# Optimization experiments

Measured on AMD Instinct MI355X. Metric: run time of the kernel, lower is better.

Reference implementation:

```python
import jax, jax.numpy as jnp
import numpy as np

B, L, D_IN, D_H, D_OUT = 8, 1024, 1024, 1024, 1024


def setup_inputs() -> dict:
    key = jax.random.key(0)
    ks = jax.random.split(key, 9)
    s = 0.02  # weight scale to keep ReLU chain stable
    return {
        "leaves": jax.random.normal(ks[0], (B, L, D_IN), dtype=jnp.float32),
        "V_w": jax.random.normal(ks[1], (D_H, D_IN), dtype=jnp.float32) * s,
        "V_b": jax.random.normal(ks[2], (D_H,), dtype=jnp.float32) * s,
        "U_w": jax.random.normal(ks[3], (D_H, D_H), dtype=jnp.float32) * s,
        "U_b": jax.random.normal(ks[4], (D_H,), dtype=jnp.float32) * s,
        "W_w": jax.random.normal(ks[5], (D_H, D_H), dtype=jnp.float32) * s,
        "W_b": jax.random.normal(ks[6], (D_H,), dtype=jnp.float32) * s,
        "O_w": jax.random.normal(ks[7], (D_OUT, D_H), dtype=jnp.float32) * s,
        "O_b": jax.random.normal(ks[8], (D_OUT,), dtype=jnp.float32) * s,
    }


def reference(leaves, V_w, V_b, U_w, U_b, W_w, W_b, O_w, O_b):
    # Leaf encoding: h_leaf = relu(V(x))            [B, L, H]
    h = jax.nn.relu(jnp.einsum("bli,hi->blh", leaves, V_w) + V_b)
    # Depth-batched recursion over the complete binary tree:
    # combined = relu(U(left) + W(right)); log2(L) levels, node count halves.
    while h.shape[1] > 1:
        left, right = h[:, 0::2], h[:, 1::2]  # [B, n/2, H] each
        h = jax.nn.relu(
            jnp.einsum("bnh,gh->bng", left, U_w) + U_b
            + jnp.einsum("bnh,gh->bng", right, W_w) + W_b
        )
    root = h[:, 0]  # [B, H]
    logits = jnp.einsum("bh,oh->bo", root, O_w) + O_b
    return jax.nn.log_softmax(logits, axis=-1)
```

## Files before the change

### kernel.cpp

```cpp
#include <hip/hip_runtime.h>
#include <hip/hip_bf16.h>
#include <math.h>

typedef __bf16 bf16_t;
typedef __bf16 bf16x8 __attribute__((ext_vector_type(8)));
typedef __bf16 bf16x4 __attribute__((ext_vector_type(4)));
typedef float  f32x4  __attribute__((ext_vector_type(4)));

#define GLD_LDS16(g, l)                                                          \
  __builtin_amdgcn_global_load_lds((const __attribute__((address_space(1))) void*)(g), \
                                   (__attribute__((address_space(3))) void*)(l), 16, 0, 0)

__global__ __launch_bounds__(256) void k_cvt_all(const float* __restrict__ leaves,
                                                 const float* __restrict__ V_w,
                                                 const float* __restrict__ O_w,
                                                 const float* __restrict__ U_w,
                                                 const float* __restrict__ W_w,
                                                 const float* __restrict__ U_b,
                                                 const float* __restrict__ W_b,
                                                 bf16_t* __restrict__ leaves_bf,
                                                 bf16_t* __restrict__ Vw_bf,
                                                 bf16_t* __restrict__ Ow_bf,
                                                 bf16_t* __restrict__ UW_bf,
                                                 float* __restrict__ buw) {
  const int gtid = blockIdx.x * 256 + threadIdx.x;
  const int G = gridDim.x * 256;
  for (int i = gtid; i < 2097152; i += G) {
    float4 v = reinterpret_cast<const float4*>(leaves)[i];
    bf16x4 o; o[0] = (bf16_t)v.x; o[1] = (bf16_t)v.y; o[2] = (bf16_t)v.z; o[3] = (bf16_t)v.w;
    reinterpret_cast<bf16x4*>(leaves_bf)[i] = o;
  }
  for (int i = gtid; i < 262144; i += G) {
    float4 v = reinterpret_cast<const float4*>(V_w)[i];
    bf16x4 o; o[0] = (bf16_t)v.x; o[1] = (bf16_t)v.y; o[2] = (bf16_t)v.z; o[3] = (bf16_t)v.w;
    reinterpret_cast<bf16x4*>(Vw_bf)[i] = o;
  }
  for (int i = gtid; i < 262144; i += G) {
    float4 v = reinterpret_cast<const float4*>(O_w)[i];
    bf16x4 o; o[0] = (bf16_t)v.x; o[1] = (bf16_t)v.y; o[2] = (bf16_t)v.z; o[3] = (bf16_t)v.w;
    reinterpret_cast<bf16x4*>(Ow_bf)[i] = o;
  }
  for (int idx = gtid; idx < 524288; idx += G) {
    int i = idx * 4;
    int g = i >> 11;
    int k = i & 2047;
    const float* src = (k < 1024) ? (U_w + g * 1024 + k) : (W_w + g * 1024 + (k - 1024));
    float4 v = *reinterpret_cast<const float4*>(src);
    bf16x4 o; o[0] = (bf16_t)v.x; o[1] = (bf16_t)v.y; o[2] = (bf16_t)v.z; o[3] = (bf16_t)v.w;
    reinterpret_cast<bf16x4*>(UW_bf)[idx] = o;
  }
  if (gtid < 1024) buw[gtid] = U_b[gtid] + W_b[gtid];
}

template <int TM, int TN, bool SPLIT>
__global__ __launch_bounds__(256, (TM == 128 ? 2 : 3)) void k_gemm(
    const bf16_t* __restrict__ A, const bf16_t* __restrict__ Bw,
    const float* __restrict__ bias, bf16_t* __restrict__ C,
    bf16_t* __restrict__ P, int M, int Kstride, int kchunk) {
  constexpr int MI = TM / 32;
  constexpr int NJ = TN / 32;
  constexpr int VM = TM / 64 + TN / 64;
  constexpr int NB = (TM == 128 ? 5 : 4);
  __shared__ bf16_t As[NB][TM * 32];
  __shared__ bf16_t Bs[NB][TN * 32];

  const int tid = threadIdx.x;
  const int lane = tid & 63;
  const int wave = tid >> 6;
  const int wr = wave >> 1, wc = wave & 1;
  const int bm = blockIdx.x, bn = blockIdx.y, bz = blockIdx.z;

  const bf16_t* Abase = A + (size_t)bm * TM * Kstride + (size_t)bz * kchunk;
  const bf16_t* Bbase = Bw + (size_t)bn * TN * Kstride + (size_t)bz * kchunk;

  f32x4 acc[MI][NJ] = {};
  const int rl = lane & 15, kq = lane >> 4;

  auto stage = [&](int buf, int ko) {
#pragma unroll
    for (int it = 0; it < TM / 64; ++it) {
      int c = tid + 256 * it;
      int r = c >> 2, kbp = c & 3;
      int kb = kbp ^ ((r >> 1) & 3);
      GLD_LDS16(Abase + (size_t)r * Kstride + ko + kb * 8, &As[buf][c * 8]);
    }
#pragma unroll
    for (int it = 0; it < TN / 64; ++it) {
      int c = tid + 256 * it;
      int r = c >> 2, kbp = c & 3;
      int kb = kbp ^ ((r >> 1) & 3);
      GLD_LDS16(Bbase + (size_t)r * Kstride + ko + kb * 8, &Bs[buf][c * 8]);
    }
  };

  const int kiters = kchunk >> 5;
  stage(0, 0);
  if (kiters > 1) stage(1, 32);
  if (kiters > 2) stage(2, 64);
  if (NB >= 5 && kiters > 3) stage(3, 96);

  int cur = 0;
  for (int t = 0; t < kiters; ++t) {
    const int nin = kiters - 1 - t;
    if (NB >= 5 && nin >= 3)
      asm volatile("s_waitcnt vmcnt(%0)" :: "i"(3 * VM) : "memory");
    else if (nin >= 2)
      asm volatile("s_waitcnt vmcnt(%0)" :: "i"(2 * VM) : "memory");
    else if (nin == 1)
      asm volatile("s_waitcnt vmcnt(%0)" :: "i"(VM) : "memory");
    else
      asm volatile("s_waitcnt vmcnt(0)" ::: "memory");
    __builtin_amdgcn_s_barrier();
    __builtin_amdgcn_sched_barrier(0);
    if (t + NB - 1 < kiters) {
      int bnx = cur + NB - 1; if (bnx >= NB) bnx -= NB;
      stage(bnx, (t + NB - 1) * 32);
    }
    bf16x8 af[MI], bfr[NJ];
#pragma unroll
    for (int i = 0; i < MI; ++i) {
      int r = wr * (TM / 2) + i * 16 + rl;
      int kbp = kq ^ ((r >> 1) & 3);
      af[i] = *reinterpret_cast<const bf16x8*>(&As[cur][r * 32 + kbp * 8]);
    }
#pragma unroll
    for (int j = 0; j < NJ; ++j) {
      int r = wc * (TN / 2) + j * 16 + rl;
      int kbp = kq ^ ((r >> 1) & 3);
      bfr[j] = *reinterpret_cast<const bf16x8*>(&Bs[cur][r * 32 + kbp * 8]);
    }
#pragma unroll
    for (int i = 0; i < MI; ++i)
#pragma unroll
      for (int j = 0; j < NJ; ++j)
        acc[i][j] = __builtin_amdgcn_mfma_f32_16x16x32_bf16(af[i], bfr[j], acc[i][j], 0, 0, 0);
    if (++cur >= NB) cur = 0;
  }

  const int rq = lane >> 4, cl = lane & 15;
  if (SPLIT) {
    bf16_t* Pp = P + (size_t)bz * M * 1024;
#pragma unroll
    for (int j = 0; j < NJ; ++j) {
      int gcol = bn * TN + wc * (TN / 2) + j * 16 + cl;
#pragma unroll
      for (int i = 0; i < MI; ++i) {
        int grow = bm * TM + wr * (TM / 2) + i * 16 + rq * 4;
#pragma unroll
        for (int reg = 0; reg < 4; ++reg)
          if (grow + reg < M)
            Pp[(size_t)(grow + reg) * 1024 + gcol] = (bf16_t)acc[i][j][reg];
      }
    }
  } else {
#pragma unroll
    for (int j = 0; j < NJ; ++j) {
      int gcol = bn * TN + wc * (TN / 2) + j * 16 + cl;
      float bv = bias[gcol];
#pragma unroll
      for (int i = 0; i < MI; ++i) {
        int grow = bm * TM + wr * (TM / 2) + i * 16 + rq * 4;
#pragma unroll
        for (int reg = 0; reg < 4; ++reg) {
          float v = acc[i][j][reg] + bv;
          v = v > 0.0f ? v : 0.0f;
          C[(size_t)(grow + reg) * 1024 + gcol] = (bf16_t)v;
        }
      }
    }
  }
}

__global__ __launch_bounds__(256) void k_reduce(const bf16_t* __restrict__ P,
                                                const float* __restrict__ bias,
                                                bf16_t* __restrict__ C, int M, int ks) {
  constexpr int N = 1024;
  int idx = blockIdx.x * 256 + threadIdx.x;
  int col = (idx * 4) & (N - 1);
  int row = (idx * 4) >> 10;
  float s0 = 0.0f, s1 = 0.0f, s2 = 0.0f, s3 = 0.0f;
  for (int z = 0; z < ks; ++z) {
    bf16x4 v = *reinterpret_cast<const bf16x4*>(P + ((size_t)z * M + row) * N + col);
    s0 += (float)v[0]; s1 += (float)v[1]; s2 += (float)v[2]; s3 += (float)v[3];
  }
  float4 b = *reinterpret_cast<const float4*>(bias + col);
  bf16x4 o;
  o[0] = (bf16_t)fmaxf(s0 + b.x, 0.0f);
  o[1] = (bf16_t)fmaxf(s1 + b.y, 0.0f);
  o[2] = (bf16_t)fmaxf(s2 + b.z, 0.0f);
  o[3] = (bf16_t)fmaxf(s3 + b.w, 0.0f);
  reinterpret_cast<bf16x4*>(C)[idx] = o;
}

template <int KK, bool RELU, bool F32OUT>
__global__ __launch_bounds__(256) void k_tail(const bf16_t* __restrict__ A,
                                              const bf16_t* __restrict__ Bw,
                                              const float* __restrict__ bias,
                                              void* __restrict__ Cout, int M) {
  constexpr int N = 1024;
  constexpr int KPL = KK / 64;
  const int lane = threadIdx.x & 63;
  const int gw = blockIdx.x * 4 + (threadIdx.x >> 6);
  const int n = gw & (N - 1);
  const int mbase = (gw >> 10) * 8;
  const int k0 = lane * KPL;

  float bv[KPL];
  const bf16_t* bp = Bw + (size_t)n * KK + k0;
#pragma unroll
  for (int q = 0; q < KPL / 8; ++q) {
    bf16x8 v = *reinterpret_cast<const bf16x8*>(bp + q * 8);
#pragma unroll
    for (int j = 0; j < 8; ++j) bv[q * 8 + j] = (float)v[j];
  }

  float acc[8];
#pragma unroll
  for (int m = 0; m < 8; ++m) {
    const bf16_t* ap = A + (size_t)(mbase + m) * KK + k0;
    float s = 0.0f;
#pragma unroll
    for (int q = 0; q < KPL / 8; ++q) {
      bf16x8 v = *reinterpret_cast<const bf16x8*>(ap + q * 8);
#pragma unroll
      for (int j = 0; j < 8; ++j) s += (float)v[j] * bv[q * 8 + j];
    }
    acc[m] = s;
  }
#pragma unroll
  for (int m = 0; m < 8; ++m) {
#pragma unroll
    for (int off = 32; off >= 1; off >>= 1) acc[m] += __shfl_xor(acc[m], off, 64);
  }
  if (lane < 8 && mbase + lane < M) {
    float v = acc[lane] + bias[n];
    if (RELU) v = v > 0.0f ? v : 0.0f;
    if (F32OUT) ((float*)Cout)[(size_t)(mbase + lane) * N + n] = v;
    else        ((bf16_t*)Cout)[(size_t)(mbase + lane) * N + n] = (bf16_t)v;
  }
}

__global__ __launch_bounds__(256) void k_logsoftmax(const float* __restrict__ logits,
                                                    float* __restrict__ out) {
  int b = blockIdx.x;
  const float* x = logits + b * 1024;
  int tid = threadIdx.x;
  int wave = tid >> 6, lane = tid & 63;
  __shared__ float red[8];

  float m = -1e30f;
  for (int i = tid; i < 1024; i += 256) m = fmaxf(m, x[i]);
#pragma unroll
  for (int off = 32; off >= 1; off >>= 1) m = fmaxf(m, __shfl_xor(m, off, 64));
  if (lane == 0) red[wave] = m;
  __syncthreads();
  m = fmaxf(fmaxf(red[0], red[1]), fmaxf(red[2], red[3]));
  float s = 0.0f;
  for (int i = tid; i < 1024; i += 256) s += expf(x[i] - m);
#pragma unroll
  for (int off = 32; off >= 1; off >>= 1) s += __shfl_xor(s, off, 64);
  if (lane == 0) red[wave] = s;
  __syncthreads();
  float lse = m + logf(red[0] + red[1] + red[2] + red[3]);
  for (int i = tid; i < 1024; i += 256) out[b * 1024 + i] = x[i] - lse;
}

extern "C" void kernel_launch(void* const* d_in, const int* in_sizes, int n_in,
                              void* d_out, int out_size, void* d_ws, size_t ws_size,
                              hipStream_t stream) {
  const float* leaves = (const float*)d_in[0];
  const float* V_w = (const float*)d_in[1];
  const float* V_b = (const float*)d_in[2];
  const float* U_w = (const float*)d_in[3];
  const float* U_b = (const float*)d_in[4];
  const float* W_w = (const float*)d_in[5];
  const float* W_b = (const float*)d_in[6];
  const float* O_w = (const float*)d_in[7];
  const float* O_b = (const float*)d_in[8];
  float* out = (float*)d_out;

  char* ws = (char*)d_ws;
  size_t off = 0;
  auto alloc = [&](size_t bytes) -> void* {
    off = (off + 255) & ~(size_t)255;
    void* p = ws + off;
    off += bytes;
    return p;
  };

  const size_t MB16 = (size_t)8192 * 1024 * 2;
  bf16_t* leaves_bf = (bf16_t*)alloc(MB16);
  bf16_t* Vw_bf = (bf16_t*)alloc((size_t)1024 * 1024 * 2);
  bf16_t* UW_bf = (bf16_t*)alloc((size_t)2 * 1024 * 1024 * 2);
  bf16_t* Ow_bf = (bf16_t*)alloc((size_t)1024 * 1024 * 2);
  float* buw = (float*)alloc(1024 * 4);
  bf16_t* hA = (bf16_t*)alloc(MB16);
  float* logits = (float*)alloc(8 * 1024 * 4);
  bf16_t* Pbuf = (bf16_t*)alloc((size_t)8 * 4096 * 1024 * 2);
  (void)ws_size; (void)in_sizes; (void)n_in; (void)out_size;

  k_cvt_all<<<2048, 256, 0, stream>>>(leaves, V_w, O_w, U_w, W_w, U_b, W_b,
                                      leaves_bf, Vw_bf, Ow_bf, UW_bf, buw);

  k_gemm<128, 128, false><<<dim3(64, 8), 256, 0, stream>>>(
      leaves_bf, Vw_bf, V_b, hA, nullptr, 8192, 1024, 1024);

  bf16_t* src = hA;
  bf16_t* dst = leaves_bf;
  auto swap = [&]() { bf16_t* t = src; src = dst; dst = t; };

  k_gemm<128, 128, true><<<dim3(32, 8, 2), 256, 0, stream>>>(
      src, UW_bf, nullptr, nullptr, Pbuf, 4096, 2048, 1024);
  k_reduce<<<4096 * 1024 / 4 / 256, 256, 0, stream>>>(Pbuf, buw, dst, 4096, 2);
  swap();
  k_gemm<64, 128, true><<<dim3(32, 8, 2), 256, 0, stream>>>(
      src, UW_bf, nullptr, nullptr, Pbuf, 2048, 2048, 1024);
  k_reduce<<<2048 * 1024 / 4 / 256, 256, 0, stream>>>(Pbuf, buw, dst, 2048, 2);
  swap();
  k_gemm<64, 128, true><<<dim3(16, 8, 4), 256, 0, stream>>>(
      src, UW_bf, nullptr, nullptr, Pbuf, 1024, 2048, 512);
  k_reduce<<<1024 * 1024 / 4 / 256, 256, 0, stream>>>(Pbuf, buw, dst, 1024, 4);
  swap();
  k_gemm<64, 128, true><<<dim3(8, 8, 4), 256, 0, stream>>>(
      src, UW_bf, nullptr, nullptr, Pbuf, 512, 2048, 512);
  k_reduce<<<512 * 1024 / 4 / 256, 256, 0, stream>>>(Pbuf, buw, dst, 512, 4);
  swap();
  k_gemm<64, 128, true><<<dim3(4, 8, 8), 256, 0, stream>>>(
      src, UW_bf, nullptr, nullptr, Pbuf, 256, 2048, 256);
  k_reduce<<<256 * 1024 / 4 / 256, 256, 0, stream>>>(Pbuf, buw, dst, 256, 8);
  swap();
  k_gemm<64, 128, true><<<dim3(2, 8, 8), 256, 0, stream>>>(
      src, UW_bf, nullptr, nullptr, Pbuf, 128, 2048, 256);
  k_reduce<<<128 * 1024 / 4 / 256, 256, 0, stream>>>(Pbuf, buw, dst, 128, 8);
  swap();
  k_gemm<64, 128, true><<<dim3(1, 8, 16), 256, 0, stream>>>(
      src, UW_bf, nullptr, nullptr, Pbuf, 64, 2048, 128);
  k_reduce<<<64 * 1024 / 4 / 256, 256, 0, stream>>>(Pbuf, buw, dst, 64, 16);
  swap();
  k_gemm<64, 128, true><<<dim3(1, 8, 16), 256, 0, stream>>>(
      src, UW_bf, nullptr, nullptr, Pbuf, 32, 2048, 128);
  k_reduce<<<32 * 1024 / 4 / 256, 256, 0, stream>>>(Pbuf, buw, dst, 32, 16);
  swap();
  for (int M = 16; M >= 8; M >>= 1) {
    int blocks = (M / 8) * 1024 / 4;
    k_tail<2048, true, false><<<blocks, 256, 0, stream>>>(src, UW_bf, buw, dst, M);
    swap();
  }

  k_tail<1024, false, true><<<256, 256, 0, stream>>>(src, Ow_bf, O_b, logits, 8);
  k_logsoftmax<<<8, 256, 0, stream>>>(logits, out);
}
```

Before: 199.8 us.

## Add 512-thread 8-wave GEMM for large levels and drop split-K at level two

Adds a k_gemm2 kernel with 512 threads (8 waves in a 2x4 layout) over a 128x128 tile, with a 5-deep LDS pipeline. It is used for the leaf encoding and the first tree level, giving each wave a smaller per-wave tile and more waves per block to hide latency. The second tree level now runs as a single non-split GEMM with fused bias and ReLU, removing the partial-sum buffer write and the separate reduce kernel. The old kernel is fixed to a 4-buffer pipeline with 3 blocks per CU. The trade-off is register and LDS pressure in the new kernel, and less parallelism at level two without split-K.

```diff
diff --git a/kernel.cpp b/kernel.cpp
--- a/kernel.cpp
+++ b/kernel.cpp
@@ -52,15 +52,126 @@
   if (gtid < 1024) buw[gtid] = U_b[gtid] + W_b[gtid];
 }
 
+template <bool SPLIT>
+__global__ __launch_bounds__(512, 4) void k_gemm2(
+    const bf16_t* __restrict__ A, const bf16_t* __restrict__ Bw,
+    const float* __restrict__ bias, bf16_t* __restrict__ C,
+    bf16_t* __restrict__ P, int M, int Kstride, int kchunk) {
+  constexpr int NB = 5;
+  constexpr int VM = 2;
+  __shared__ bf16_t As[NB][128 * 32];
+  __shared__ bf16_t Bs[NB][128 * 32];
+
+  const int tid = threadIdx.x;
+  const int lane = tid & 63;
+  const int wave = tid >> 6;
+  const int wr = wave >> 2;
+  const int wc = wave & 3;
+  const int bm = blockIdx.x, bn = blockIdx.y, bz = blockIdx.z;
+
+  const bf16_t* Abase = A + (size_t)bm * 128 * Kstride + (size_t)bz * kchunk;
+  const bf16_t* Bbase = Bw + (size_t)bn * 128 * Kstride + (size_t)bz * kchunk;
+
+  f32x4 acc[4][2] = {};
+  const int rl = lane & 15, kq = lane >> 4;
+
+  auto stage = [&](int buf, int ko) {
+    {
+      int c = tid;
+      int r = c >> 2, kbp = c & 3;
+      int kb = kbp ^ ((r >> 1) & 3);
+      GLD_LDS16(Abase + (size_t)r * Kstride + ko + kb * 8, &As[buf][c * 8]);
+    }
+    {
+      int c = tid;
+      int r = c >> 2, kbp = c & 3;
+      int kb = kbp ^ ((r >> 1) & 3);
+      GLD_LDS16(Bbase + (size_t)r * Kstride + ko + kb * 8, &Bs[buf][c * 8]);
+    }
+  };
+
+  const int kiters = kchunk >> 5;
+  stage(0, 0);
+  if (kiters > 1) stage(1, 32);
+  if (kiters > 2) stage(2, 64);
+  if (kiters > 3) stage(3, 96);
+
+  int cur = 0;
+  for (int t = 0; t < kiters; ++t) {
+    const int nin = kiters - 1 - t;
+    if (nin >= 3)      asm volatile("s_waitcnt vmcnt(%0)" :: "i"(3 * VM) : "memory");
+    else if (nin == 2) asm volatile("s_waitcnt vmcnt(%0)" :: "i"(2 * VM) : "memory");
+    else if (nin == 1) asm volatile("s_waitcnt vmcnt(%0)" :: "i"(VM) : "memory");
+    else               asm volatile("s_waitcnt vmcnt(0)" ::: "memory");
+    __builtin_amdgcn_s_barrier();
+    __builtin_amdgcn_sched_barrier(0);
+    if (t + NB - 1 < kiters) {
+      int bnx = cur + NB - 1; if (bnx >= NB) bnx -= NB;
+      stage(bnx, (t + NB - 1) * 32);
+    }
+    bf16x8 af[4], bfr[2];
+#pragma unroll
+    for (int i = 0; i < 4; ++i) {
+      int r = wr * 64 + i * 16 + rl;
+      int kbp = kq ^ ((r >> 1) & 3);
+      af[i] = *reinterpret_cast<const bf16x8*>(&As[cur][r * 32 + kbp * 8]);
+    }
+#pragma unroll
+    for (int j = 0; j < 2; ++j) {
+      int r = wc * 32 + j * 16 + rl;
+      int kbp = kq ^ ((r >> 1) & 3);
+      bfr[j] = *reinterpret_cast<const bf16x8*>(&Bs[cur][r * 32 + kbp * 8]);
+    }
+#pragma unroll
+    for (int i = 0; i < 4; ++i)
+#pragma unroll
+      for (int j = 0; j < 2; ++j)
+        acc[i][j] = __builtin_amdgcn_mfma_f32_16x16x32_bf16(af[i], bfr[j], acc[i][j], 0, 0, 0);
+    if (++cur >= NB) cur = 0;
+  }
+
+  const int rq = lane >> 4, cl = lane & 15;
+  if (SPLIT) {
+    bf16_t* Pp = P + (size_t)bz * M * 1024;
+#pragma unroll
+    for (int j = 0; j < 2; ++j) {
+      int gcol = bn * 128 + wc * 32 + j * 16 + cl;
+#pragma unroll
+      for (int i = 0; i < 4; ++i) {
+        int grow = bm * 128 + wr * 64 + i * 16 + rq * 4;
+#pragma unroll
+        for (int reg = 0; reg < 4; ++reg)
+          Pp[(size_t)(grow + reg) * 1024 + gcol] = (bf16_t)acc[i][j][reg];
+      }
+    }
+  } else {
+#pragma unroll
+    for (int j = 0; j < 2; ++j) {
+      int gcol = bn * 128 + wc * 32 + j * 16 + cl;
+      float bv = bias[gcol];
+#pragma unroll
+      for (int i = 0; i < 4; ++i) {
+        int grow = bm * 128 + wr * 64 + i * 16 + rq * 4;
+#pragma unroll
+        for (int reg = 0; reg < 4; ++reg) {
+          float v = acc[i][j][reg] + bv;
+          v = v > 0.0f ? v : 0.0f;
+          C[(size_t)(grow + reg) * 1024 + gcol] = (bf16_t)v;
+        }
+      }
+    }
+  }
+}
+
 template <int TM, int TN, bool SPLIT>
-__global__ __launch_bounds__(256, (TM == 128 ? 2 : 3)) void k_gemm(
+__global__ __launch_bounds__(256, 3) void k_gemm(
     const bf16_t* __restrict__ A, const bf16_t* __restrict__ Bw,
     const float* __restrict__ bias, bf16_t* __restrict__ C,
     bf16_t* __restrict__ P, int M, int Kstride, int kchunk) {
   constexpr int MI = TM / 32;
   constexpr int NJ = TN / 32;
   constexpr int VM = TM / 64 + TN / 64;
-  constexpr int NB = (TM == 128 ? 5 : 4);
+  constexpr int NB = 4;
   __shared__ bf16_t As[NB][TM * 32];
   __shared__ bf16_t Bs[NB][TN * 32];
 
@@ -97,19 +208,13 @@
   stage(0, 0);
   if (kiters > 1) stage(1, 32);
   if (kiters > 2) stage(2, 64);
-  if (NB >= 5 && kiters > 3) stage(3, 96);
 
   int cur = 0;
   for (int t = 0; t < kiters; ++t) {
     const int nin = kiters - 1 - t;
-    if (NB >= 5 && nin >= 3)
-      asm volatile("s_waitcnt vmcnt(%0)" :: "i"(3 * VM) : "memory");
-    else if (nin >= 2)
-      asm volatile("s_waitcnt vmcnt(%0)" :: "i"(2 * VM) : "memory");
-    else if (nin == 1)
-      asm volatile("s_waitcnt vmcnt(%0)" :: "i"(VM) : "memory");
-    else
-      asm volatile("s_waitcnt vmcnt(0)" ::: "memory");
+    if (nin >= 2)      asm volatile("s_waitcnt vmcnt(%0)" :: "i"(2 * VM) : "memory");
+    else if (nin == 1) asm volatile("s_waitcnt vmcnt(%0)" :: "i"(VM) : "memory");
+    else               asm volatile("s_waitcnt vmcnt(0)" ::: "memory");
     __builtin_amdgcn_s_barrier();
     __builtin_amdgcn_sched_barrier(0);
     if (t + NB - 1 < kiters) {
@@ -302,20 +407,19 @@
   k_cvt_all<<<2048, 256, 0, stream>>>(leaves, V_w, O_w, U_w, W_w, U_b, W_b,
                                       leaves_bf, Vw_bf, Ow_bf, UW_bf, buw);
 
-  k_gemm<128, 128, false><<<dim3(64, 8), 256, 0, stream>>>(
+  k_gemm2<false><<<dim3(64, 8), 512, 0, stream>>>(
       leaves_bf, Vw_bf, V_b, hA, nullptr, 8192, 1024, 1024);
 
   bf16_t* src = hA;
   bf16_t* dst = leaves_bf;
   auto swap = [&]() { bf16_t* t = src; src = dst; dst = t; };
 
-  k_gemm<128, 128, true><<<dim3(32, 8, 2), 256, 0, stream>>>(
+  k_gemm2<true><<<dim3(32, 8, 2), 512, 0, stream>>>(
       src, UW_bf, nullptr, nullptr, Pbuf, 4096, 2048, 1024);
   k_reduce<<<4096 * 1024 / 4 / 256, 256, 0, stream>>>(Pbuf, buw, dst, 4096, 2);
   swap();
-  k_gemm<64, 128, true><<<dim3(32, 8, 2), 256, 0, stream>>>(
-      src, UW_bf, nullptr, nullptr, Pbuf, 2048, 2048, 1024);
-  k_reduce<<<2048 * 1024 / 4 / 256, 256, 0, stream>>>(Pbuf, buw, dst, 2048, 2);
+  k_gemm<64, 128, false><<<dim3(32, 8), 256, 0, stream>>>(
+      src, UW_bf, buw, dst, nullptr, 2048, 2048, 2048);
   swap();
   k_gemm<64, 128, true><<<dim3(16, 8, 4), 256, 0, stream>>>(
       src, UW_bf, nullptr, nullptr, Pbuf, 1024, 2048, 512);
```

New measurement: 203.0 us. About the same (+1.6%).
